# Kernel optimization log

Hardware: AMD Instinct MI355X
Metric: run time of the kernel (lower is better)

Reference implementation:

```python
import jax, jax.numpy as jnp
import numpy as np

B, N, D = 2, 2048, 768
H = 12
DH = D // H
SCALE = DH ** -0.5


def setup_inputs() -> dict:
    key = jax.random.key(0)
    k1, k2, k3 = jax.random.split(key, 3)
    x = jax.random.normal(k1, (B, N, D), dtype=jnp.float32)
    w_qkv = jax.random.normal(k2, (D, 3 * D), dtype=jnp.float32) * (D ** -0.5)
    b_qkv = jnp.zeros((3 * D,), dtype=jnp.float32)
    w_proj = jax.random.normal(k3, (D, D), dtype=jnp.float32) * (D ** -0.5)
    b_proj = jnp.zeros((D,), dtype=jnp.float32)
    return {"x": x, "w_qkv": w_qkv, "b_qkv": b_qkv, "w_proj": w_proj, "b_proj": b_proj}


def reference(x, w_qkv, b_qkv, w_proj, b_proj):
    b, n, d = x.shape
    # qkv: (B, n, 3, H, DH) -> (3, B, H, n, DH)
    qkv = (x @ w_qkv + b_qkv).reshape(b, n, 3, H, DH).transpose(2, 0, 3, 1, 4)
    q, k, v = qkv[0], qkv[1], qkv[2]
    # naive full attention matrix (B, H, n, n)
    attn = jnp.einsum('bhqd,bhkd->bhqk', q, k) * SCALE
    attn = jax.nn.softmax(attn, axis=-1)
    out = jnp.einsum('bhqk,bhkd->bhqd', attn, v)  # (B, H, n, DH)
    out = out.transpose(0, 2, 1, 3).reshape(b, n, d)
    return out @ w_proj + b_proj
```

## Files before the change

### kernel.cpp

```cpp
#include <hip/hip_runtime.h>


#define CB 2
#define CN 2048
#define CD 768
#define CH 12
#define CDH 64
#define CEXPSCALE 0.18033688f

typedef __bf16 bf16x8 __attribute__((ext_vector_type(8)));
typedef float f32x4 __attribute__((ext_vector_type(4)));
typedef unsigned short u16x8 __attribute__((ext_vector_type(8)));

static __device__ __forceinline__ unsigned short f2bf(float f) {
  union { float f; unsigned u; } v; v.f = f;
  unsigned r = v.u + 0x7fffu + ((v.u >> 16) & 1u);
  return (unsigned short)(r >> 16);
}

static __device__ __forceinline__ void gld_lds16(const unsigned short* g, unsigned short* lds_base) {
  __builtin_amdgcn_global_load_lds(
      (const __attribute__((address_space(1))) unsigned int*)g,
      (__attribute__((address_space(3))) unsigned int*)(unsigned int)(unsigned long long)lds_base,
      16, 0, 0);
}

__global__ __launch_bounds__(256) void prep(const float* __restrict__ x,
                                            unsigned short* __restrict__ xb,
                                            const float* __restrict__ w_qkv,
                                            unsigned short* __restrict__ wqkv_t,
                                            const float* __restrict__ w_proj,
                                            unsigned short* __restrict__ wproj_t) {
  __shared__ __align__(16) unsigned short t[64][72];
  const int bid = blockIdx.x, tid = threadIdx.x;
#pragma unroll
  for (int it = 0; it < 2; ++it) {
    size_t i = ((size_t)(bid * 2 + it) * 256 + tid) * 8;
    f32x4 a = *(const f32x4*)&x[i];
    f32x4 b = *(const f32x4*)&x[i + 4];
    u16x8 o;
#pragma unroll
    for (int j = 0; j < 4; ++j) { o[j] = f2bf(a[j]); o[4 + j] = f2bf(b[j]); }
    *(u16x8*)&xb[i] = o;
  }
  if (bid >= 576) return;
  const float* src; unsigned short* dst; int R, C, c0, r0;
  if (bid < 432) { src = w_qkv; dst = wqkv_t; R = 768; C = 2304; c0 = (bid % 36) * 64; r0 = (bid / 36) * 64; }
  else { int u = bid - 432; src = w_proj; dst = wproj_t; R = 768; C = 768; c0 = (u % 12) * 64; r0 = (u / 12) * 64; }
#pragma unroll
  for (int i = 0; i < 4; ++i) {
    int c = tid + i * 256;
    int row = c >> 4, cc = (c & 15) * 4;
    f32x4 v = *(const f32x4*)&src[(size_t)(r0 + row) * C + c0 + cc];
#pragma unroll
    for (int j = 0; j < 4; ++j) t[row][cc + j] = f2bf(v[j]);
  }
  __syncthreads();
#pragma unroll
  for (int i = 0; i < 2; ++i) {
    int c = tid + i * 256;
    int drow = c >> 3, rc = (c & 7) * 8;
    u16x8 v;
#pragma unroll
    for (int j = 0; j < 8; ++j) v[j] = t[rc + j][drow];
    *(u16x8*)&dst[(size_t)(c0 + drow) * R + r0 + rc] = v;
  }
}

extern __shared__ __align__(16) unsigned short smem[];

template <int TM, int TN>
__global__ __launch_bounds__(256, 4) void gemm_db(const unsigned short* __restrict__ A,
                                                  const unsigned short* __restrict__ Bt,
                                                  const float* __restrict__ bias,
                                                  int M, int N, int K, int mode,
                                                  unsigned short* __restrict__ o0,
                                                  unsigned short* __restrict__ o1,
                                                  unsigned short* __restrict__ o2,
                                                  float* __restrict__ outF) {
  constexpr int NT = TN / 32;
  unsigned short* As = smem;
  unsigned short* Bs = smem + 2 * TM * 32;
  unsigned short* Ct = smem;
  const int tid = threadIdx.x;
  const int w = tid >> 6, lane = tid & 63, quad = lane >> 4, lc = lane & 15;
  const int wm = (w >> 1) * 32, wn = (w & 1) * (TN / 2);
  const int row0 = blockIdx.y * TM, col0 = blockIdx.x * TN;
  f32x4 acc[2][NT] = {};

  const int rl = lane >> 2, cl = lane & 3;
  const int gc = cl ^ ((rl >> 1) & 3);
  const int rsw = (lc >> 1) & 3;
  const int nk = K / 32;

  auto stage = [&](int kt, int buf) {
    const int k0 = kt * 32;
    gld_lds16(&A[(size_t)(row0 + w * 16 + rl) * K + k0 + gc * 8],
              &As[buf * (TM * 32) + (w * 16) * 32]);
#pragma unroll
    for (int jb = 0; jb < TN / 64; ++jb)
      gld_lds16(&Bt[(size_t)(col0 + w * (TN / 4) + jb * 16 + rl) * K + k0 + gc * 8],
                &Bs[buf * (TN * 32) + (w * (TN / 4) + jb * 16) * 32]);
  };

  stage(0, 0);
  for (int kt = 0; kt < nk; ++kt) {
    const int bb = kt & 1;
    __syncthreads();
    if (kt + 1 < nk) stage(kt + 1, bb ^ 1);
    bf16x8 af[2], bfv[NT];
#pragma unroll
    for (int mt = 0; mt < 2; ++mt)
      af[mt] = *(const bf16x8*)&As[bb * (TM * 32) + (wm + mt * 16 + lc) * 32 + (quad ^ rsw) * 8];
#pragma unroll
    for (int nt = 0; nt < NT; ++nt)
      bfv[nt] = *(const bf16x8*)&Bs[bb * (TN * 32) + (wn + nt * 16 + lc) * 32 + (quad ^ rsw) * 8];
#pragma unroll
    for (int mt = 0; mt < 2; ++mt)
#pragma unroll
      for (int nt = 0; nt < NT; ++nt)
        acc[mt][nt] = __builtin_amdgcn_mfma_f32_16x16x32_bf16(af[mt], bfv[nt], acc[mt][nt], 0, 0, 0);
  }

  if (mode == 0 && col0 >= 1536) {
    __syncthreads();
#pragma unroll
    for (int mt = 0; mt < 2; ++mt) {
#pragma unroll
      for (int nt = 0; nt < NT; ++nt) {
        int jl = wn + nt * 16 + lc;
        int il0 = wm + mt * 16 + quad * 4;
        float bj = bias[col0 + jl];
        unsigned short a0 = f2bf(acc[mt][nt][0] + bj);
        unsigned short a1 = f2bf(acc[mt][nt][1] + bj);
        unsigned short a2 = f2bf(acc[mt][nt][2] + bj);
        unsigned short a3 = f2bf(acc[mt][nt][3] + bj);
        uint2 dd;
        dd.x = (unsigned)a0 | ((unsigned)a1 << 16);
        dd.y = (unsigned)a2 | ((unsigned)a3 << 16);
        *(uint2*)&Ct[jl * (TM + 8) + il0] = dd;
      }
    }
    __syncthreads();
    const int b = row0 >> 11, n0 = row0 & 2047;
    constexpr int CPR = TM / 8;
#pragma unroll
    for (int i = 0; i < (TN * CPR) / 256; ++i) {
      int c = tid + i * 256;
      int jl = c / CPR, cc = (c % CPR) * 8;
      u16x8 v = *(const u16x8*)&Ct[jl * (TM + 8) + cc];
      int jcol = col0 - 1536 + jl;
      int h = jcol >> 6, d = jcol & 63;
      size_t gr = ((size_t)(b * CH + h) * CDH + d);
      *(u16x8*)&o2[gr * CN + n0 + cc] = v;
    }
  } else {
#pragma unroll
    for (int mt = 0; mt < 2; ++mt) {
#pragma unroll
      for (int nt = 0; nt < NT; ++nt) {
#pragma unroll
        for (int r = 0; r < 4; ++r) {
          int i = row0 + wm + mt * 16 + quad * 4 + r;
          int j = col0 + wn + nt * 16 + lc;
          float v = acc[mt][nt][r] + bias[j];
          if (mode == 0) {
            int b = i >> 11, n = i & 2047;
            int sec = (j >= 768) ? 1 : 0;
            int within = j - sec * 768;
            int h = within >> 6, d = within & 63;
            int bh = b * CH + h;
            if (sec == 0) o0[((size_t)bh * CN + n) * CDH + d] = f2bf(v * CEXPSCALE);
            else          o1[((size_t)bh * CN + n) * CDH + d] = f2bf(v);
          } else {
            outF[(size_t)i * N + j] = v;
          }
        }
      }
    }
  }
}

__global__ __launch_bounds__(256, 3) void attn64(const unsigned short* __restrict__ Q,
                                                 const unsigned short* __restrict__ K,
                                                 const unsigned short* __restrict__ Vt,
                                                 unsigned short* __restrict__ O) {
  __shared__ __align__(16) unsigned short Kls[2][64 * 64];
  __shared__ __align__(16) unsigned short Vls[2][64 * 64];
  const int bh = blockIdx.x, qt0 = blockIdx.y;
  const int tid = threadIdx.x;
  const int w = tid >> 6, lane = tid & 63, quad = lane >> 4, lc = lane & 15;
  const unsigned short* Qb = Q + (size_t)bh * CN * CDH;
  const unsigned short* Kb = K + (size_t)bh * CN * CDH;
  const unsigned short* Vb = Vt + (size_t)bh * CDH * CN;
  const int q0w = qt0 * 64 + w * 16;

  const int sr = lane >> 3, sc = lane & 7;
  const int sg = sc ^ sr;
  const int ksw = lc & 7;
  const int c0 = (quad ^ ksw) * 8;
  const int c1 = ((4 | quad) ^ ksw) * 8;

  int ks[2];
#pragma unroll
  for (int j2 = 0; j2 < 2; ++j2) {
    int s = (w * 2 + j2) * 8 + sr;
    ks[j2] = ((s & 28) << 1) | ((s & 32) >> 3) | (s & 3);
  }

  bf16x8 qf[2];
#pragma unroll
  for (int hh = 0; hh < 2; ++hh)
    qf[hh] = *(const bf16x8*)&Qb[(size_t)(q0w + lc) * CDH + hh * 32 + quad * 8];

  f32x4 o[4] = {};
  float rs = 0.f;

  union PU { unsigned u[4]; bf16x8 v; } P0p, P1p;
  P0p.u[0] = P0p.u[1] = P0p.u[2] = P0p.u[3] = 0;
  P1p = P0p;
  bf16x8 vfp[4][2];
#pragma unroll
  for (int dt = 0; dt < 4; ++dt) { vfp[dt][0] = P0p.v; vfp[dt][1] = P0p.v; }

#pragma unroll
  for (int j2 = 0; j2 < 2; ++j2) {
    int j = w * 2 + j2;
    int r = j * 8 + sr;
    gld_lds16(&Kb[(size_t)ks[j2] * CDH + sg * 8], &Kls[0][j * 8 * 64]);
    gld_lds16(&Vb[(size_t)r * CN + 0 + sg * 8], &Vls[0][j * 8 * 64]);
  }

  for (int kt = 0; kt < CN / 64; ++kt) {
    const int bb = kt & 1;
    __syncthreads();
    if (kt + 1 < CN / 64) {
      const int kn = (kt + 1) * 64;
#pragma unroll
      for (int j2 = 0; j2 < 2; ++j2) {
        int j = w * 2 + j2;
        int r = j * 8 + sr;
        gld_lds16(&Kb[(size_t)(kn + ks[j2]) * CDH + sg * 8], &Kls[bb ^ 1][j * 8 * 64]);
        gld_lds16(&Vb[(size_t)r * CN + kn + sg * 8], &Vls[bb ^ 1][j * 8 * 64]);
      }
    }
    __builtin_amdgcn_s_setprio(1);
#pragma unroll
    for (int dt = 0; dt < 4; ++dt) {
      o[dt] = __builtin_amdgcn_mfma_f32_16x16x32_bf16(P0p.v, vfp[dt][0], o[dt], 0, 0, 0);
      o[dt] = __builtin_amdgcn_mfma_f32_16x16x32_bf16(P1p.v, vfp[dt][1], o[dt], 0, 0, 0);
    }
    __builtin_amdgcn_s_setprio(0);
    bf16x8 kf[4][2];
#pragma unroll
    for (int kvt = 0; kvt < 4; ++kvt) {
      const int row = (kvt * 16 + lc) * 64;
      kf[kvt][0] = *(const bf16x8*)&Kls[bb][row + c0];
      kf[kvt][1] = *(const bf16x8*)&Kls[bb][row + c1];
    }
    f32x4 z[4] = {};
    __builtin_amdgcn_s_setprio(1);
#pragma unroll
    for (int kvt = 0; kvt < 4; ++kvt) {
      z[kvt] = __builtin_amdgcn_mfma_f32_16x16x32_bf16(kf[kvt][0], qf[0], z[kvt], 0, 0, 0);
      z[kvt] = __builtin_amdgcn_mfma_f32_16x16x32_bf16(kf[kvt][1], qf[1], z[kvt], 0, 0, 0);
    }
    __builtin_amdgcn_s_setprio(0);
#pragma unroll
    for (int dt = 0; dt < 4; ++dt) {
      const int row = (dt * 16 + lc) * 64;
      vfp[dt][0] = *(const bf16x8*)&Vls[bb][row + c0];
      vfp[dt][1] = *(const bf16x8*)&Vls[bb][row + c1];
    }
#pragma unroll
    for (int g = 0; g < 2; ++g) {
      unsigned pu[4];
#pragma unroll
      for (int hpair = 0; hpair < 2; ++hpair) {
        const int kvt = hpair * 2 + g;
        float e0 = __builtin_amdgcn_exp2f(z[kvt][0]);
        float e1 = __builtin_amdgcn_exp2f(z[kvt][1]);
        float e2 = __builtin_amdgcn_exp2f(z[kvt][2]);
        float e3 = __builtin_amdgcn_exp2f(z[kvt][3]);
        rs += (e0 + e1) + (e2 + e3);
        pu[hpair * 2]     = __builtin_amdgcn_perm(__float_as_uint(e1), __float_as_uint(e0), 0x07060302u);
        pu[hpair * 2 + 1] = __builtin_amdgcn_perm(__float_as_uint(e3), __float_as_uint(e2), 0x07060302u);
      }
      if (g == 0) { P0p.u[0] = pu[0]; P0p.u[1] = pu[1]; P0p.u[2] = pu[2]; P0p.u[3] = pu[3]; }
      else        { P1p.u[0] = pu[0]; P1p.u[1] = pu[1]; P1p.u[2] = pu[2]; P1p.u[3] = pu[3]; }
    }
  }

  __builtin_amdgcn_s_setprio(1);
#pragma unroll
  for (int dt = 0; dt < 4; ++dt) {
    o[dt] = __builtin_amdgcn_mfma_f32_16x16x32_bf16(P0p.v, vfp[dt][0], o[dt], 0, 0, 0);
    o[dt] = __builtin_amdgcn_mfma_f32_16x16x32_bf16(P1p.v, vfp[dt][1], o[dt], 0, 0, 0);
  }
  __builtin_amdgcn_s_setprio(0);

  rs += __shfl_xor(rs, 16, 64);
  rs += __shfl_xor(rs, 32, 64);
  const int b = bh / CH, h = bh - b * CH;
#pragma unroll
  for (int r = 0; r < 4; ++r) {
    float lr = __shfl(rs, quad * 4 + r, 64);
    float inv = 1.0f / lr;
    int i = b * CN + q0w + quad * 4 + r;
#pragma unroll
    for (int dt = 0; dt < 4; ++dt) {
      int j = h * CDH + dt * 16 + lc;
      O[(size_t)i * CD + j] = f2bf(o[dt][r] * inv);
    }
  }
}

extern "C" void kernel_launch(void* const* d_in, const int* in_sizes, int n_in,
                              void* d_out, int out_size, void* d_ws, size_t ws_size,
                              hipStream_t stream) {
  const float* x      = (const float*)d_in[0];
  const float* w_qkv  = (const float*)d_in[1];
  const float* b_qkv  = (const float*)d_in[2];
  const float* w_proj = (const float*)d_in[3];
  const float* b_proj = (const float*)d_in[4];
  float* out = (float*)d_out;
  unsigned short* ws = (unsigned short*)d_ws;

  unsigned short* xb      = ws;
  unsigned short* wqkv_t  = xb + (size_t)4096 * 768;
  unsigned short* wproj_t = wqkv_t + (size_t)2304 * 768;
  unsigned short* Qs  = wproj_t + (size_t)768 * 768;
  unsigned short* Ks  = Qs  + (size_t)CB * CH * CN * CDH;
  unsigned short* Vts = Ks  + (size_t)CB * CH * CN * CDH;
  unsigned short* AO  = Vts + (size_t)CB * CH * CN * CDH;

  const size_t smem_qkv  = (size_t)2 * (64 + 128) * 32 * 2;
  const size_t smem_proj = (size_t)2 * (64 + 64) * 32 * 2;

  prep<<<768, 256, 0, stream>>>(x, xb, w_qkv, wqkv_t, w_proj, wproj_t);
  gemm_db<64, 128><<<dim3(2304 / 128, 4096 / 64), 256, smem_qkv, stream>>>(
      xb, wqkv_t, b_qkv, 4096, 2304, 768, 0, Qs, Ks, Vts, nullptr);
  attn64<<<dim3(CB * CH, CN / 64), 256, 0, stream>>>(Qs, Ks, Vts, AO);
  gemm_db<64, 64><<<dim3(768 / 64, 4096 / 64), 256, smem_proj, stream>>>(
      AO, wproj_t, b_proj, 4096, 768, 768, 1, nullptr, nullptr, nullptr, out);
}
```

Before: 159.8 us.

## Process two query tiles per wave in attention to reuse K/V fragments

The attention kernel now runs with 2 waves per block instead of 4, and each wave handles 32 query rows (two 16-row tiles) instead of 16. The K and V fragments read from LDS are reused across both query tiles, which halves LDS reads per MFMA. Each wave also issues twice as many global-to-LDS loads per tile. The cost is higher register pressure (double accumulators, Q fragments and P buffers) and fewer waves per block, with launch bounds changed to 128 threads and 2 blocks.

After: 162.3 us. About the same (+1.6%).

```diff
diff --git a/kernel.cpp b/kernel.cpp
--- a/kernel.cpp
+++ b/kernel.cpp
@@ -181,7 +181,7 @@
   }
 }
 
-__global__ __launch_bounds__(256, 3) void attn64(const unsigned short* __restrict__ Q,
+__global__ __launch_bounds__(128, 2) void attn64(const unsigned short* __restrict__ Q,
                                                  const unsigned short* __restrict__ K,
                                                  const unsigned short* __restrict__ Vt,
                                                  unsigned short* __restrict__ O) {
@@ -193,7 +193,7 @@
   const unsigned short* Qb = Q + (size_t)bh * CN * CDH;
   const unsigned short* Kb = K + (size_t)bh * CN * CDH;
   const unsigned short* Vb = Vt + (size_t)bh * CDH * CN;
-  const int q0w = qt0 * 64 + w * 16;
+  const int q0w = qt0 * 64 + w * 32;
 
   const int sr = lane >> 3, sc = lane & 7;
   const int sg = sc ^ sr;
@@ -201,31 +201,33 @@
   const int c0 = (quad ^ ksw) * 8;
   const int c1 = ((4 | quad) ^ ksw) * 8;
 
-  int ks[2];
-#pragma unroll
-  for (int j2 = 0; j2 < 2; ++j2) {
-    int s = (w * 2 + j2) * 8 + sr;
+  int ks[4];
+#pragma unroll
+  for (int j2 = 0; j2 < 4; ++j2) {
+    int s = (w * 4 + j2) * 8 + sr;
     ks[j2] = ((s & 28) << 1) | ((s & 32) >> 3) | (s & 3);
   }
 
-  bf16x8 qf[2];
-#pragma unroll
-  for (int hh = 0; hh < 2; ++hh)
-    qf[hh] = *(const bf16x8*)&Qb[(size_t)(q0w + lc) * CDH + hh * 32 + quad * 8];
-
-  f32x4 o[4] = {};
-  float rs = 0.f;
-
-  union PU { unsigned u[4]; bf16x8 v; } P0p, P1p;
-  P0p.u[0] = P0p.u[1] = P0p.u[2] = P0p.u[3] = 0;
-  P1p = P0p;
+  bf16x8 qf[2][2];
+#pragma unroll
+  for (int qt = 0; qt < 2; ++qt)
+#pragma unroll
+    for (int hh = 0; hh < 2; ++hh)
+      qf[qt][hh] = *(const bf16x8*)&Qb[(size_t)(q0w + qt * 16 + lc) * CDH + hh * 32 + quad * 8];
+
+  f32x4 o[2][4] = {};
+  float rs0 = 0.f, rs1 = 0.f;
+
+  union PU { unsigned u[4]; bf16x8 v; } P[2][2];
+  P[0][0].u[0] = P[0][0].u[1] = P[0][0].u[2] = P[0][0].u[3] = 0;
+  P[0][1] = P[0][0]; P[1][0] = P[0][0]; P[1][1] = P[0][0];
   bf16x8 vfp[4][2];
 #pragma unroll
-  for (int dt = 0; dt < 4; ++dt) { vfp[dt][0] = P0p.v; vfp[dt][1] = P0p.v; }
-
-#pragma unroll
-  for (int j2 = 0; j2 < 2; ++j2) {
-    int j = w * 2 + j2;
+  for (int dt = 0; dt < 4; ++dt) { vfp[dt][0] = P[0][0].v; vfp[dt][1] = P[0][0].v; }
+
+#pragma unroll
+  for (int j2 = 0; j2 < 4; ++j2) {
+    int j = w * 4 + j2;
     int r = j * 8 + sr;
     gld_lds16(&Kb[(size_t)ks[j2] * CDH + sg * 8], &Kls[0][j * 8 * 64]);
     gld_lds16(&Vb[(size_t)r * CN + 0 + sg * 8], &Vls[0][j * 8 * 64]);
@@ -237,8 +239,8 @@
     if (kt + 1 < CN / 64) {
       const int kn = (kt + 1) * 64;
 #pragma unroll
-      for (int j2 = 0; j2 < 2; ++j2) {
-        int j = w * 2 + j2;
+      for (int j2 = 0; j2 < 4; ++j2) {
+        int j = w * 4 + j2;
         int r = j * 8 + sr;
         gld_lds16(&Kb[(size_t)(kn + ks[j2]) * CDH + sg * 8], &Kls[bb ^ 1][j * 8 * 64]);
         gld_lds16(&Vb[(size_t)r * CN + kn + sg * 8], &Vls[bb ^ 1][j * 8 * 64]);
@@ -246,10 +248,12 @@
     }
     __builtin_amdgcn_s_setprio(1);
 #pragma unroll
-    for (int dt = 0; dt < 4; ++dt) {
-      o[dt] = __builtin_amdgcn_mfma_f32_16x16x32_bf16(P0p.v, vfp[dt][0], o[dt], 0, 0, 0);
-      o[dt] = __builtin_amdgcn_mfma_f32_16x16x32_bf16(P1p.v, vfp[dt][1], o[dt], 0, 0, 0);
-    }
+    for (int qt = 0; qt < 2; ++qt)
+#pragma unroll
+      for (int dt = 0; dt < 4; ++dt) {
+        o[qt][dt] = __builtin_amdgcn_mfma_f32_16x16x32_bf16(P[qt][0].v, vfp[dt][0], o[qt][dt], 0, 0, 0);
+        o[qt][dt] = __builtin_amdgcn_mfma_f32_16x16x32_bf16(P[qt][1].v, vfp[dt][1], o[qt][dt], 0, 0, 0);
+      }
     __builtin_amdgcn_s_setprio(0);
     bf16x8 kf[4][2];
 #pragma unroll
@@ -258,13 +262,15 @@
       kf[kvt][0] = *(const bf16x8*)&Kls[bb][row + c0];
       kf[kvt][1] = *(const bf16x8*)&Kls[bb][row + c1];
     }
-    f32x4 z[4] = {};
+    f32x4 z[2][4] = {};
     __builtin_amdgcn_s_setprio(1);
 #pragma unroll
-    for (int kvt = 0; kvt < 4; ++kvt) {
-      z[kvt] = __builtin_amdgcn_mfma_f32_16x16x32_bf16(kf[kvt][0], qf[0], z[kvt], 0, 0, 0);
-      z[kvt] = __builtin_amdgcn_mfma_f32_16x16x32_bf16(kf[kvt][1], qf[1], z[kvt], 0, 0, 0);
-    }
+    for (int kvt = 0; kvt < 4; ++kvt)
+#pragma unroll
+      for (int qt = 0; qt < 2; ++qt) {
+        z[qt][kvt] = __builtin_amdgcn_mfma_f32_16x16x32_bf16(kf[kvt][0], qf[qt][0], z[qt][kvt], 0, 0, 0);
+        z[qt][kvt] = __builtin_amdgcn_mfma_f32_16x16x32_bf16(kf[kvt][1], qf[qt][1], z[qt][kvt], 0, 0, 0);
+      }
     __builtin_amdgcn_s_setprio(0);
 #pragma unroll
     for (int dt = 0; dt < 4; ++dt) {
@@ -273,44 +279,52 @@
       vfp[dt][1] = *(const bf16x8*)&Vls[bb][row + c1];
     }
 #pragma unroll
-    for (int g = 0; g < 2; ++g) {
-      unsigned pu[4];
-#pragma unroll
-      for (int hpair = 0; hpair < 2; ++hpair) {
-        const int kvt = hpair * 2 + g;
-        float e0 = __builtin_amdgcn_exp2f(z[kvt][0]);
-        float e1 = __builtin_amdgcn_exp2f(z[kvt][1]);
-        float e2 = __builtin_amdgcn_exp2f(z[kvt][2]);
-        float e3 = __builtin_amdgcn_exp2f(z[kvt][3]);
-        rs += (e0 + e1) + (e2 + e3);
-        pu[hpair * 2]     = __builtin_amdgcn_perm(__float_as_uint(e1), __float_as_uint(e0), 0x07060302u);
-        pu[hpair * 2 + 1] = __builtin_amdgcn_perm(__float_as_uint(e3), __float_as_uint(e2), 0x07060302u);
-      }
-      if (g == 0) { P0p.u[0] = pu[0]; P0p.u[1] = pu[1]; P0p.u[2] = pu[2]; P0p.u[3] = pu[3]; }
-      else        { P1p.u[0] = pu[0]; P1p.u[1] = pu[1]; P1p.u[2] = pu[2]; P1p.u[3] = pu[3]; }
-    }
+    for (int qt = 0; qt < 2; ++qt)
+#pragma unroll
+      for (int g = 0; g < 2; ++g) {
+        unsigned pu[4];
+#pragma unroll
+        for (int hpair = 0; hpair < 2; ++hpair) {
+          const int kvt = hpair * 2 + g;
+          float e0 = __builtin_amdgcn_exp2f(z[qt][kvt][0]);
+          float e1 = __builtin_amdgcn_exp2f(z[qt][kvt][1]);
+          float e2 = __builtin_amdgcn_exp2f(z[qt][kvt][2]);
+          float e3 = __builtin_amdgcn_exp2f(z[qt][kvt][3]);
+          if (qt == 0) rs0 += (e0 + e1) + (e2 + e3);
+          else         rs1 += (e0 + e1) + (e2 + e3);
+          pu[hpair * 2]     = __builtin_amdgcn_perm(__float_as_uint(e1), __float_as_uint(e0), 0x07060302u);
+          pu[hpair * 2 + 1] = __builtin_amdgcn_perm(__float_as_uint(e3), __float_as_uint(e2), 0x07060302u);
+        }
+        P[qt][g].u[0] = pu[0]; P[qt][g].u[1] = pu[1];
+        P[qt][g].u[2] = pu[2]; P[qt][g].u[3] = pu[3];
+      }
   }
 
   __builtin_amdgcn_s_setprio(1);
 #pragma unroll
-  for (int dt = 0; dt < 4; ++dt) {
-    o[dt] = __builtin_amdgcn_mfma_f32_16x16x32_bf16(P0p.v, vfp[dt][0], o[dt], 0, 0, 0);
-    o[dt] = __builtin_amdgcn_mfma_f32_16x16x32_bf16(P1p.v, vfp[dt][1], o[dt], 0, 0, 0);
-  }
+  for (int qt = 0; qt < 2; ++qt)
+#pragma unroll
+    for (int dt = 0; dt < 4; ++dt) {
+      o[qt][dt] = __builtin_amdgcn_mfma_f32_16x16x32_bf16(P[qt][0].v, vfp[dt][0], o[qt][dt], 0, 0, 0);
+      o[qt][dt] = __builtin_amdgcn_mfma_f32_16x16x32_bf16(P[qt][1].v, vfp[dt][1], o[qt][dt], 0, 0, 0);
+    }
   __builtin_amdgcn_s_setprio(0);
 
-  rs += __shfl_xor(rs, 16, 64);
-  rs += __shfl_xor(rs, 32, 64);
+  rs0 += __shfl_xor(rs0, 16, 64); rs0 += __shfl_xor(rs0, 32, 64);
+  rs1 += __shfl_xor(rs1, 16, 64); rs1 += __shfl_xor(rs1, 32, 64);
   const int b = bh / CH, h = bh - b * CH;
 #pragma unroll
-  for (int r = 0; r < 4; ++r) {
-    float lr = __shfl(rs, quad * 4 + r, 64);
-    float inv = 1.0f / lr;
-    int i = b * CN + q0w + quad * 4 + r;
-#pragma unroll
-    for (int dt = 0; dt < 4; ++dt) {
-      int j = h * CDH + dt * 16 + lc;
-      O[(size_t)i * CD + j] = f2bf(o[dt][r] * inv);
+  for (int qt = 0; qt < 2; ++qt) {
+#pragma unroll
+    for (int r = 0; r < 4; ++r) {
+      float lr = __shfl(qt == 0 ? rs0 : rs1, quad * 4 + r, 64);
+      float inv = 1.0f / lr;
+      int i = b * CN + q0w + qt * 16 + quad * 4 + r;
+#pragma unroll
+      for (int dt = 0; dt < 4; ++dt) {
+        int j = h * CDH + dt * 16 + lc;
+        O[(size_t)i * CD + j] = f2bf(o[qt][dt][r] * inv);
+      }
     }
   }
 }
@@ -340,7 +354,7 @@
   prep<<<768, 256, 0, stream>>>(x, xb, w_qkv, wqkv_t, w_proj, wproj_t);
   gemm_db<64, 128><<<dim3(2304 / 128, 4096 / 64), 256, smem_qkv, stream>>>(
       xb, wqkv_t, b_qkv, 4096, 2304, 768, 0, Qs, Ks, Vts, nullptr);
-  attn64<<<dim3(CB * CH, CN / 64), 256, 0, stream>>>(Qs, Ks, Vts, AO);
+  attn64<<<dim3(CB * CH, CN / 64), 128, 0, stream>>>(Qs, Ks, Vts, AO);
   gemm_db<64, 64><<<dim3(768 / 64, 4096 / 64), 256, smem_proj, stream>>>(
       AO, wproj_t, b_proj, 4096, 768, 768, 1, nullptr, nullptr, nullptr, out);
 }
```

## Triple-buffer K/V LDS tiles with explicit vmcnt waits in attention loop

Applied to the files above, without the earlier changes.

Switches the attention kernel's K/V shared-memory staging from double to triple buffering, prefetching two tiles ahead. It replaces the plain __syncthreads with an explicit s_waitcnt vmcnt(4) plus s_barrier, so only the oldest tile's async global-to-LDS loads must be complete. The aim is to hide more global load latency behind the MFMA work. The cost is 50% more LDS per block, which may lower occupancy at the requested 3 blocks per SM, and the hand-written waitcnt counts are fragile.

Result: no change. 158.4 us (-0.9%).

```diff
diff --git a/kernel.cpp b/kernel.cpp
--- a/kernel.cpp
+++ b/kernel.cpp
@@ -185,8 +185,8 @@
                                                  const unsigned short* __restrict__ K,
                                                  const unsigned short* __restrict__ Vt,
                                                  unsigned short* __restrict__ O) {
-  __shared__ __align__(16) unsigned short Kls[2][64 * 64];
-  __shared__ __align__(16) unsigned short Vls[2][64 * 64];
+  __shared__ __align__(16) unsigned short Kls[3][64 * 64];
+  __shared__ __align__(16) unsigned short Vls[3][64 * 64];
   const int bh = blockIdx.x, qt0 = blockIdx.y;
   const int tid = threadIdx.x;
   const int w = tid >> 6, lane = tid & 63, quad = lane >> 4, lc = lane & 15;
@@ -208,6 +208,16 @@
     ks[j2] = ((s & 28) << 1) | ((s & 32) >> 3) | (s & 3);
   }
 
+  auto stageT = [&](int kn, int buf) {
+#pragma unroll
+    for (int j2 = 0; j2 < 2; ++j2) {
+      int j = w * 2 + j2;
+      int r = j * 8 + sr;
+      gld_lds16(&Kb[(size_t)(kn + ks[j2]) * CDH + sg * 8], &Kls[buf][j * 8 * 64]);
+      gld_lds16(&Vb[(size_t)r * CN + kn + sg * 8], &Vls[buf][j * 8 * 64]);
+    }
+  };
+
   bf16x8 qf[2];
 #pragma unroll
   for (int hh = 0; hh < 2; ++hh)
@@ -223,26 +233,18 @@
 #pragma unroll
   for (int dt = 0; dt < 4; ++dt) { vfp[dt][0] = P0p.v; vfp[dt][1] = P0p.v; }
 
-#pragma unroll
-  for (int j2 = 0; j2 < 2; ++j2) {
-    int j = w * 2 + j2;
-    int r = j * 8 + sr;
-    gld_lds16(&Kb[(size_t)ks[j2] * CDH + sg * 8], &Kls[0][j * 8 * 64]);
-    gld_lds16(&Vb[(size_t)r * CN + 0 + sg * 8], &Vls[0][j * 8 * 64]);
-  }
-
-  for (int kt = 0; kt < CN / 64; ++kt) {
-    const int bb = kt & 1;
-    __syncthreads();
-    if (kt + 1 < CN / 64) {
-      const int kn = (kt + 1) * 64;
-#pragma unroll
-      for (int j2 = 0; j2 < 2; ++j2) {
-        int j = w * 2 + j2;
-        int r = j * 8 + sr;
-        gld_lds16(&Kb[(size_t)(kn + ks[j2]) * CDH + sg * 8], &Kls[bb ^ 1][j * 8 * 64]);
-        gld_lds16(&Vb[(size_t)r * CN + kn + sg * 8], &Vls[bb ^ 1][j * 8 * 64]);
-      }
+  constexpr int nk = CN / 64;
+  stageT(0, 0);
+  stageT(64, 1);
+
+  int cur = 0;
+  for (int kt = 0; kt < nk; ++kt) {
+    if (kt < nk - 1) asm volatile("s_waitcnt vmcnt(4)" ::: "memory");
+    else             asm volatile("s_waitcnt vmcnt(0)" ::: "memory");
+    __builtin_amdgcn_s_barrier();
+    if (kt + 2 < nk) {
+      int st = (cur == 0) ? 2 : cur - 1;
+      stageT((kt + 2) * 64, st);
     }
     __builtin_amdgcn_s_setprio(1);
 #pragma unroll
@@ -255,8 +257,8 @@
 #pragma unroll
     for (int kvt = 0; kvt < 4; ++kvt) {
       const int row = (kvt * 16 + lc) * 64;
-      kf[kvt][0] = *(const bf16x8*)&Kls[bb][row + c0];
-      kf[kvt][1] = *(const bf16x8*)&Kls[bb][row + c1];
+      kf[kvt][0] = *(const bf16x8*)&Kls[cur][row + c0];
+      kf[kvt][1] = *(const bf16x8*)&Kls[cur][row + c1];
     }
     f32x4 z[4] = {};
     __builtin_amdgcn_s_setprio(1);
@@ -269,8 +271,8 @@
 #pragma unroll
     for (int dt = 0; dt < 4; ++dt) {
       const int row = (dt * 16 + lc) * 64;
-      vfp[dt][0] = *(const bf16x8*)&Vls[bb][row + c0];
-      vfp[dt][1] = *(const bf16x8*)&Vls[bb][row + c1];
+      vfp[dt][0] = *(const bf16x8*)&Vls[cur][row + c0];
+      vfp[dt][1] = *(const bf16x8*)&Vls[cur][row + c1];
     }
 #pragma unroll
     for (int g = 0; g < 2; ++g) {
@@ -289,6 +291,7 @@
       if (g == 0) { P0p.u[0] = pu[0]; P0p.u[1] = pu[1]; P0p.u[2] = pu[2]; P0p.u[3] = pu[3]; }
       else        { P1p.u[0] = pu[0]; P1p.u[1] = pu[1]; P1p.u[2] = pu[2]; P1p.u[3] = pu[3]; }
     }
+    cur = (cur == 2) ? 0 : cur + 1;
   }
 
   __builtin_amdgcn_s_setprio(1);
```
